# Kernel tuning notes

Hardware: AMD Instinct MI355X
Metric: run time of the kernel (lower is better)

## Reference

```python
import jax, jax.numpy as jnp
import numpy as np

EPS = 1e-5


def setup_inputs() -> dict:
    key = jax.random.key(0)
    ks = jax.random.split(key, 5)
    N, E, D, L = 10000, 160000, 512, 3
    x = jax.random.normal(ks[0], (N, D), dtype=jnp.float32)
    src = jax.random.randint(ks[1], (E,), 0, N, dtype=jnp.int64)
    dst = jax.random.randint(ks[2], (E,), 0, N, dtype=jnp.int64)
    gamma = jnp.ones((L, D), dtype=jnp.float32)
    beta = jnp.zeros((L, D), dtype=jnp.float32)
    # glorot-ish scale so ReLU stack stays well-conditioned
    W = jax.random.normal(ks[3], (L, D, D), dtype=jnp.float32) * (1.0 / np.sqrt(D))
    b = jnp.zeros((L, D), dtype=jnp.float32)
    return {"x": x, "src": src, "dst": dst, "gamma": gamma, "beta": beta, "W": W, "b": b}


def reference(x, src, dst, gamma, beta, W, b):
    N = x.shape[0]
    ones = jnp.ones(src.shape[0], dtype=x.dtype)
    # DGL GraphConv norm='both': src side uses out-degree, dst side uses in-degree
    out_deg = jnp.clip(jax.ops.segment_sum(ones, src, num_segments=N), 1.0)
    in_deg = jnp.clip(jax.ops.segment_sum(ones, dst, num_segments=N), 1.0)
    src_norm = (out_deg ** -0.5)[:, None]  # [N,1]
    dst_norm = (in_deg ** -0.5)[:, None]   # [N,1]
    n_layers = gamma.shape[0]
    for i in range(n_layers):
        # BatchNorm1d (training mode: batch mean, biased variance)
        mu = jnp.mean(x, axis=0)
        var = jnp.var(x, axis=0)
        x = (x - mu) * jax.lax.rsqrt(var + EPS) * gamma[i] + beta[i]
        h = x * src_norm
        agg = jax.ops.segment_sum(h[src], dst, num_segments=N) * dst_norm
        x = jax.nn.relu(agg @ W[i] + b[i])
    return x
```

## Files before the change

### kernel.cpp

```cpp
#include <hip/hip_runtime.h>
#include <hip/hip_bf16.h>

constexpr int N = 10000;
constexpr int D = 512;
constexpr int E = 160000;
constexpr int L = 3;
constexpr float EPS = 1e-5f;

typedef _Float16 half8 __attribute__((ext_vector_type(8)));
typedef float floatx4 __attribute__((ext_vector_type(4)));

__global__ void compute_degrees(const int* __restrict__ src,
                                const int* __restrict__ dst,
                                int* __restrict__ out_deg,
                                int* __restrict__ in_deg) {
    int e = blockIdx.x * blockDim.x + threadIdx.x;
    if (e >= E) return;
    atomicAdd(&out_deg[src[e]], 1);
    atomicAdd(&in_deg[dst[e]], 1);
}

__global__ void scan_indeg(const int* __restrict__ in_deg,
                           const int* __restrict__ out_deg,
                           int* __restrict__ off, int* __restrict__ cursor,
                           float* __restrict__ src_norm, float* __restrict__ dst_norm) {
    __shared__ int lsum[1024];
    int t = threadIdx.x;
    const int chunk = (N + 1023) / 1024;
    int start = t * chunk;
    int end = start + chunk; if (end > N) end = N;
    int s = 0;
    for (int i = start; i < end; ++i) s += in_deg[i];
    lsum[t] = s;
    __syncthreads();
    for (int d = 1; d < 1024; d <<= 1) {
        int v = (t >= d) ? lsum[t - d] : 0;
        __syncthreads();
        lsum[t] += v;
        __syncthreads();
    }
    int excl = (t == 0) ? 0 : lsum[t - 1];
    for (int i = start; i < end; ++i) {
        off[i] = excl;
        cursor[i] = excl;
        excl += in_deg[i];
        int od = out_deg[i]; if (od < 1) od = 1;
        int id = in_deg[i];  if (id < 1) id = 1;
        src_norm[i] = rsqrtf((float)od);
        dst_norm[i] = rsqrtf((float)id);
    }
    if (t == 1023) off[N] = lsum[1023];
}

__global__ void csr_fill(const int* __restrict__ src, const int* __restrict__ dst,
                         int* __restrict__ cursor, int* __restrict__ csr_src) {
    int e = blockIdx.x * blockDim.x + threadIdx.x;
    if (e >= E) return;
    int d = dst[e];
    int pos = atomicAdd(&cursor[d], 1);
    csr_src[pos] = src[e];
}

__global__ void transpose_W(const float* __restrict__ W, _Float16* __restrict__ Wt) {
    __shared__ float t[32][33];
    int l = blockIdx.z;
    int k0 = blockIdx.x * 32, n0 = blockIdx.y * 32;
    int tx = threadIdx.x, ty = threadIdx.y;
    const float* Wl = W + (size_t)l * D * D;
    _Float16* Wtl = Wt + (size_t)l * D * D;
    for (int i = 0; i < 32; i += 8)
        t[ty + i][tx] = Wl[(size_t)(k0 + ty + i) * D + n0 + tx];
    __syncthreads();
    for (int i = 0; i < 32; i += 8)
        Wtl[(size_t)(n0 + ty + i) * D + k0 + tx] = (_Float16)t[tx][ty + i];
}

__global__ void convert_x(const float* __restrict__ x, _Float16* __restrict__ y) {
    int i = blockIdx.x * 256 + threadIdx.x;
    if (i >= N * D / 8) return;
    const float* xp = x + (size_t)i * 8;
    half8 o;
    for (int k = 0; k < 8; ++k) o[k] = (_Float16)xp[k];
    *(half8*)(y + (size_t)i * 8) = o;
}

__global__ void col_stats(const _Float16* __restrict__ x, float* __restrict__ stats,
                          int rows_per_block) {
    int c = threadIdx.x;
    int r0 = blockIdx.x * rows_per_block;
    int r1 = r0 + rows_per_block; if (r1 > N) r1 = N;
    float s = 0.f, ss = 0.f;
    for (int r = r0; r < r1; ++r) {
        float v = (float)x[(size_t)r * D + c];
        s += v;
        ss += v * v;
    }
    atomicAdd(&stats[c], s);
    atomicAdd(&stats[D + c], ss);
}

__global__ void bn_coef(float* __restrict__ stats,
                        const float* __restrict__ gamma, const float* __restrict__ beta,
                        float* __restrict__ coef) {
    int c = threadIdx.x;
    const float invN = 1.0f / (float)N;
    float mu = stats[c] * invN;
    float var = stats[D + c] * invN - mu * mu;
    float scale = gamma[c] * rsqrtf(var + EPS);
    coef[c] = scale;
    coef[D + c] = beta[c] - mu * scale;
    stats[c] = 0.f;
    stats[D + c] = 0.f;
}

__global__ __launch_bounds__(256) void aggregate_bn(
    const _Float16* __restrict__ x, const int* __restrict__ off,
    const int* __restrict__ csr_src, const float* __restrict__ src_norm,
    const float* __restrict__ dst_norm, const float* __restrict__ coef,
    _Float16* __restrict__ agg) {
    int wid = (blockIdx.x * 256 + threadIdx.x) >> 6;
    if (wid >= N) return;
    int lane = threadIdx.x & 63;
    int c0 = lane * 8;
    int e0 = off[wid], e1 = off[wid + 1];
    float a[8] = {}, a2[8] = {};
    float t = 0.f;
    int e = e0;
    for (; e + 2 <= e1; e += 2) {
        int s0 = csr_src[e];
        int s1 = csr_src[e + 1];
        float n0 = src_norm[s0];
        float n1 = src_norm[s1];
        half8 v0 = *(const half8*)(x + (size_t)s0 * D + c0);
        half8 v1 = *(const half8*)(x + (size_t)s1 * D + c0);
        t += n0 + n1;
        for (int i = 0; i < 8; ++i) {
            a[i]  += (float)v0[i] * n0;
            a2[i] += (float)v1[i] * n1;
        }
    }
    if (e < e1) {
        int s0 = csr_src[e];
        float n0 = src_norm[s0];
        half8 v0 = *(const half8*)(x + (size_t)s0 * D + c0);
        t += n0;
        for (int i = 0; i < 8; ++i) a[i] += (float)v0[i] * n0;
    }
    float dn = dst_norm[wid];
    half8 o;
    for (int i = 0; i < 8; ++i) {
        float sc = coef[c0 + i];
        float sh = coef[D + c0 + i];
        o[i] = (_Float16)(dn * (sc * (a[i] + a2[i]) + sh * t));
    }
    *(half8*)(agg + (size_t)wid * D + c0) = o;
}

template <typename OutT, bool STATS>
__global__ __launch_bounds__(256) void mm_f16_relu(
    const _Float16* __restrict__ A, const _Float16* __restrict__ Bt,
    const float* __restrict__ bias, OutT* __restrict__ C, int M,
    float* __restrict__ stats) {
    __shared__ __align__(16) _Float16 As[128 * 32];
    __shared__ __align__(16) _Float16 Bs[128 * 32];
    const int tid  = threadIdx.x;
    const int wave = tid >> 6;
    const int lane = tid & 63;
    const int quad = lane >> 4;
    const int l16  = lane & 15;
    const int row0 = blockIdx.x * 128;
    const int col0 = blockIdx.y * 128;
    const int wm = (wave & 1) * 64;
    const int wn = (wave >> 1) * 64;

    const int sr = lane >> 2;
    const int sc = (lane & 3) * 8;

    floatx4 acc[4][4] = {};

    half8 pa[2], pb[2];
    for (int p = 0; p < 2; ++p) {
        int ar = row0 + wave * 32 + p * 16 + sr;
        if (ar >= M) ar = M - 1;
        pa[p] = *(const half8*)(A + (size_t)ar * D + sc);
        int br = col0 + wave * 32 + p * 16 + sr;
        pb[p] = *(const half8*)(Bt + (size_t)br * D + sc);
    }

    for (int k0 = 0; k0 < D; k0 += 32) {
        __syncthreads();
        for (int p = 0; p < 2; ++p) {
            int r = wave * 32 + p * 16 + sr;
            *(half8*)(As + r * 32 + sc) = pa[p];
            *(half8*)(Bs + r * 32 + sc) = pb[p];
        }
        __syncthreads();
        if (k0 + 32 < D) {
            int k1 = k0 + 32;
            for (int p = 0; p < 2; ++p) {
                int ar = row0 + wave * 32 + p * 16 + sr;
                if (ar >= M) ar = M - 1;
                pa[p] = *(const half8*)(A + (size_t)ar * D + k1 + sc);
                int br = col0 + wave * 32 + p * 16 + sr;
                pb[p] = *(const half8*)(Bt + (size_t)br * D + k1 + sc);
            }
        }
        half8 af[4], bf[4];
        for (int i = 0; i < 4; ++i)
            af[i] = *(const half8*)(As + (wm + i * 16 + l16) * 32 + quad * 8);
        for (int j = 0; j < 4; ++j)
            bf[j] = *(const half8*)(Bs + (wn + j * 16 + l16) * 32 + quad * 8);
        for (int i = 0; i < 4; ++i)
            for (int j = 0; j < 4; ++j)
                acc[i][j] = __builtin_amdgcn_mfma_f32_16x16x32_f16(af[i], bf[j], acc[i][j], 0, 0, 0);
    }

    float s[4] = {}, ss[4] = {};
    for (int i = 0; i < 4; ++i) {
        for (int r = 0; r < 4; ++r) {
            int row = row0 + wm + i * 16 + quad * 4 + r;
            bool valid = row < M;
            for (int j = 0; j < 4; ++j) {
                int col = col0 + wn + j * 16 + l16;
                float v = acc[i][j][r] + bias[col];
                v = v > 0.f ? v : 0.f;
                if (valid) {
                    C[(size_t)row * D + col] = (OutT)v;
                    if (STATS) { s[j] += v; ss[j] += v * v; }
                }
            }
        }
    }
    if (STATS) {
        for (int j = 0; j < 4; ++j) {
            float sv = s[j], qv = ss[j];
            sv += __shfl_xor(sv, 16); sv += __shfl_xor(sv, 32);
            qv += __shfl_xor(qv, 16); qv += __shfl_xor(qv, 32);
            if (quad == 0) {
                int col = col0 + wn + j * 16 + l16;
                atomicAdd(&stats[col], sv);
                atomicAdd(&stats[D + col], qv);
            }
        }
    }
}

extern "C" void kernel_launch(void* const* d_in, const int* in_sizes, int n_in,
                              void* d_out, int out_size, void* d_ws, size_t ws_size,
                              hipStream_t stream) {
    const float* x_in  = (const float*)d_in[0];
    const int*   src   = (const int*)d_in[1];
    const int*   dst   = (const int*)d_in[2];
    const float* gamma = (const float*)d_in[3];
    const float* beta  = (const float*)d_in[4];
    const float* W     = (const float*)d_in[5];
    const float* b     = (const float*)d_in[6];
    float* out = (float*)d_out;

    char* p = (char*)d_ws;
    _Float16* x16 = (_Float16*)p;  p += (size_t)N * D * 2;
    _Float16* agg = (_Float16*)p;  p += (size_t)N * D * 2;
    _Float16* Wt  = (_Float16*)p;  p += (size_t)L * D * D * 2;
    float* coef     = (float*)p;   p += 2 * D * 4;
    float* src_norm = (float*)p;   p += (size_t)N * 4;
    float* dst_norm = (float*)p;   p += (size_t)N * 4;
    int* out_deg = (int*)p;        p += (size_t)N * 4;
    int* in_deg  = (int*)p;        p += (size_t)N * 4;
    float* stats = (float*)p;      p += 2 * D * 4;
    int* csr_off = (int*)p;        p += (size_t)(N + 1) * 4;
    int* cursor  = (int*)p;        p += (size_t)N * 4;
    int* csr_src = (int*)p;        p += (size_t)E * 4;

    hipMemsetAsync(out_deg, 0, (2 * (size_t)N + 2 * D) * sizeof(int), stream);
    compute_degrees<<<(E + 255) / 256, 256, 0, stream>>>(src, dst, out_deg, in_deg);
    scan_indeg<<<1, 1024, 0, stream>>>(in_deg, out_deg, csr_off, cursor, src_norm, dst_norm);
    csr_fill<<<(E + 255) / 256, 256, 0, stream>>>(src, dst, cursor, csr_src);
    transpose_W<<<dim3(16, 16, 3), dim3(32, 8), 0, stream>>>(W, Wt);
    convert_x<<<(N * D / 8 + 255) / 256, 256, 0, stream>>>(x_in, x16);
    col_stats<<<100, D, 0, stream>>>(x16, stats, (N + 99) / 100);

    dim3 mm_grid((N + 127) / 128, D / 128);
    const int agg_blocks = (N + 3) / 4;

    for (int l = 0; l < L; ++l) {
        const float* gl  = gamma + (size_t)l * D;
        const float* bl  = beta + (size_t)l * D;
        const _Float16* Wl = Wt + (size_t)l * D * D;
        const float* bil = b + (size_t)l * D;

        bn_coef<<<1, D, 0, stream>>>(stats, gl, bl, coef);
        aggregate_bn<<<agg_blocks, 256, 0, stream>>>(x16, csr_off, csr_src,
                                                     src_norm, dst_norm, coef, agg);
        if (l == L - 1) {
            mm_f16_relu<float, false><<<mm_grid, 256, 0, stream>>>(
                agg, Wl, bil, out, N, nullptr);
        } else {
            mm_f16_relu<_Float16, true><<<mm_grid, 256, 0, stream>>>(
                agg, Wl, bil, x16, N, stats);
        }
    }
}
```

Baseline: 311.0 us.

## Fuse setup kernels, fold BN coefficients into aggregation, use direct-to-LDS GEMM loads

The degree count, x conversion with fused column stats, and W transpose now run as one combined setup kernel. Column stats are computed from the fp32 input, and per-layer stats buffers remove the bn_coef launch, since aggregation now derives the BN scale and shift inline. The GEMM tile shrinks to 128x64 and uses global_load_lds to copy tiles straight into shared memory instead of prefetching through registers. Together these cut kernel launches and register staging. The cost is that the GEMM no longer overlaps the next tile's loads with MFMA work, and the smaller tile adds grid blocks and more A re-reads.

```diff
diff --git a/kernel.cpp b/kernel.cpp
--- a/kernel.cpp
+++ b/kernel.cpp
@@ -8,16 +8,67 @@
 constexpr float EPS = 1e-5f;
 
 typedef _Float16 half8 __attribute__((ext_vector_type(8)));
+typedef _Float16 half2v __attribute__((ext_vector_type(2)));
 typedef float floatx4 __attribute__((ext_vector_type(4)));
 
-__global__ void compute_degrees(const int* __restrict__ src,
-                                const int* __restrict__ dst,
-                                int* __restrict__ out_deg,
-                                int* __restrict__ in_deg) {
-    int e = blockIdx.x * blockDim.x + threadIdx.x;
-    if (e >= E) return;
-    atomicAdd(&out_deg[src[e]], 1);
-    atomicAdd(&in_deg[dst[e]], 1);
+__device__ __forceinline__ void glds16(const _Float16* g, _Float16* l) {
+    __builtin_amdgcn_global_load_lds(
+        (const __attribute__((address_space(1))) uint32_t*)(g),
+        (__attribute__((address_space(3))) uint32_t*)(l),
+        16, 0, 0);
+}
+
+constexpr int DEG_BLOCKS  = (E + 255) / 256;
+constexpr int CONV_BLOCKS = 100;
+constexpr int TW_BLOCKS   = L * 256;
+constexpr int MEGA_BLOCKS = DEG_BLOCKS + CONV_BLOCKS + TW_BLOCKS;
+
+__global__ __launch_bounds__(256) void mega_setup(
+    const int* __restrict__ src, const int* __restrict__ dst,
+    const float* __restrict__ x, const float* __restrict__ W,
+    int* __restrict__ out_deg, int* __restrict__ in_deg,
+    _Float16* __restrict__ x16, float* __restrict__ stats0,
+    _Float16* __restrict__ Wt) {
+    __shared__ float tb[32][33];
+    int bid = blockIdx.x;
+    int tid = threadIdx.x;
+    if (bid < DEG_BLOCKS) {
+        int e = bid * 256 + tid;
+        if (e < E) {
+            atomicAdd(&out_deg[src[e]], 1);
+            atomicAdd(&in_deg[dst[e]], 1);
+        }
+    } else if (bid < DEG_BLOCKS + CONV_BLOCKS) {
+        int b = bid - DEG_BLOCKS;
+        int r0 = b * 100;
+        int r1 = r0 + 100; if (r1 > N) r1 = N;
+        int c2 = tid * 2;
+        float s0 = 0.f, s1 = 0.f, q0 = 0.f, q1 = 0.f;
+        for (int r = r0; r < r1; ++r) {
+            float2 v = *(const float2*)(x + (size_t)r * D + c2);
+            s0 += v.x; q0 += v.x * v.x;
+            s1 += v.y; q1 += v.y * v.y;
+            half2v h; h[0] = (_Float16)v.x; h[1] = (_Float16)v.y;
+            *(half2v*)(x16 + (size_t)r * D + c2) = h;
+        }
+        atomicAdd(&stats0[c2], s0);
+        atomicAdd(&stats0[c2 + 1], s1);
+        atomicAdd(&stats0[D + c2], q0);
+        atomicAdd(&stats0[D + c2 + 1], q1);
+    } else {
+        int b = bid - DEG_BLOCKS - CONV_BLOCKS;
+        int l = b >> 8;
+        int t = b & 255;
+        int k0 = (t >> 4) * 32, n0 = (t & 15) * 32;
+        int tx = tid & 31, ty = tid >> 5;
+        const float* Wl = W + (size_t)l * D * D;
+        _Float16* Wtl = Wt + (size_t)l * D * D;
+        for (int i = 0; i < 32; i += 8)
+            tb[ty + i][tx] = Wl[(size_t)(k0 + ty + i) * D + n0 + tx];
+        __syncthreads();
+        for (int i = 0; i < 32; i += 8)
+            Wtl[(size_t)(n0 + ty + i) * D + k0 + tx] = (_Float16)tb[tx][ty + i];
+    }
 }
 
 __global__ void scan_indeg(const int* __restrict__ in_deg,
@@ -61,67 +112,28 @@
     csr_src[pos] = src[e];
 }
 
-__global__ void transpose_W(const float* __restrict__ W, _Float16* __restrict__ Wt) {
-    __shared__ float t[32][33];
-    int l = blockIdx.z;
-    int k0 = blockIdx.x * 32, n0 = blockIdx.y * 32;
-    int tx = threadIdx.x, ty = threadIdx.y;
-    const float* Wl = W + (size_t)l * D * D;
-    _Float16* Wtl = Wt + (size_t)l * D * D;
-    for (int i = 0; i < 32; i += 8)
-        t[ty + i][tx] = Wl[(size_t)(k0 + ty + i) * D + n0 + tx];
-    __syncthreads();
-    for (int i = 0; i < 32; i += 8)
-        Wtl[(size_t)(n0 + ty + i) * D + k0 + tx] = (_Float16)t[tx][ty + i];
-}
-
-__global__ void convert_x(const float* __restrict__ x, _Float16* __restrict__ y) {
-    int i = blockIdx.x * 256 + threadIdx.x;
-    if (i >= N * D / 8) return;
-    const float* xp = x + (size_t)i * 8;
-    half8 o;
-    for (int k = 0; k < 8; ++k) o[k] = (_Float16)xp[k];
-    *(half8*)(y + (size_t)i * 8) = o;
-}
-
-__global__ void col_stats(const _Float16* __restrict__ x, float* __restrict__ stats,
-                          int rows_per_block) {
-    int c = threadIdx.x;
-    int r0 = blockIdx.x * rows_per_block;
-    int r1 = r0 + rows_per_block; if (r1 > N) r1 = N;
-    float s = 0.f, ss = 0.f;
-    for (int r = r0; r < r1; ++r) {
-        float v = (float)x[(size_t)r * D + c];
-        s += v;
-        ss += v * v;
-    }
-    atomicAdd(&stats[c], s);
-    atomicAdd(&stats[D + c], ss);
-}
-
-__global__ void bn_coef(float* __restrict__ stats,
-                        const float* __restrict__ gamma, const float* __restrict__ beta,
-                        float* __restrict__ coef) {
-    int c = threadIdx.x;
-    const float invN = 1.0f / (float)N;
-    float mu = stats[c] * invN;
-    float var = stats[D + c] * invN - mu * mu;
-    float scale = gamma[c] * rsqrtf(var + EPS);
-    coef[c] = scale;
-    coef[D + c] = beta[c] - mu * scale;
-    stats[c] = 0.f;
-    stats[D + c] = 0.f;
-}
-
 __global__ __launch_bounds__(256) void aggregate_bn(
     const _Float16* __restrict__ x, const int* __restrict__ off,
     const int* __restrict__ csr_src, const float* __restrict__ src_norm,
-    const float* __restrict__ dst_norm, const float* __restrict__ coef,
+    const float* __restrict__ dst_norm, const float* __restrict__ stats,
+    const float* __restrict__ gamma, const float* __restrict__ beta,
     _Float16* __restrict__ agg) {
     int wid = (blockIdx.x * 256 + threadIdx.x) >> 6;
     if (wid >= N) return;
     int lane = threadIdx.x & 63;
     int c0 = lane * 8;
+
+    float scale[8], shift[8];
+    const float invN = 1.0f / (float)N;
+    for (int i = 0; i < 8; ++i) {
+        int c = c0 + i;
+        float mu = stats[c] * invN;
+        float var = stats[D + c] * invN - mu * mu;
+        float sc = gamma[c] * rsqrtf(var + EPS);
+        scale[i] = sc;
+        shift[i] = beta[c] - mu * sc;
+    }
+
     int e0 = off[wid], e1 = off[wid + 1];
     float a[8] = {}, a2[8] = {};
     float t = 0.f;
@@ -148,11 +160,8 @@
     }
     float dn = dst_norm[wid];
     half8 o;
-    for (int i = 0; i < 8; ++i) {
-        float sc = coef[c0 + i];
-        float sh = coef[D + c0 + i];
-        o[i] = (_Float16)(dn * (sc * (a[i] + a2[i]) + sh * t));
-    }
+    for (int i = 0; i < 8; ++i)
+        o[i] = (_Float16)(dn * (scale[i] * (a[i] + a2[i]) + shift[i] * t));
     *(half8*)(agg + (size_t)wid * D + c0) = o;
 }
 
@@ -162,78 +171,67 @@
     const float* __restrict__ bias, OutT* __restrict__ C, int M,
     float* __restrict__ stats) {
     __shared__ __align__(16) _Float16 As[128 * 32];
-    __shared__ __align__(16) _Float16 Bs[128 * 32];
+    __shared__ __align__(16) _Float16 Bs[64 * 32];
     const int tid  = threadIdx.x;
     const int wave = tid >> 6;
     const int lane = tid & 63;
     const int quad = lane >> 4;
     const int l16  = lane & 15;
     const int row0 = blockIdx.x * 128;
-    const int col0 = blockIdx.y * 128;
+    const int col0 = blockIdx.y * 64;
     const int wm = (wave & 1) * 64;
-    const int wn = (wave >> 1) * 64;
-
+    const int wn = (wave >> 1) * 32;
     const int sr = lane >> 2;
     const int sc = (lane & 3) * 8;
 
-    floatx4 acc[4][4] = {};
-
-    half8 pa[2], pb[2];
-    for (int p = 0; p < 2; ++p) {
-        int ar = row0 + wave * 32 + p * 16 + sr;
-        if (ar >= M) ar = M - 1;
-        pa[p] = *(const half8*)(A + (size_t)ar * D + sc);
-        int br = col0 + wave * 32 + p * 16 + sr;
-        pb[p] = *(const half8*)(Bt + (size_t)br * D + sc);
-    }
+    int ar0 = row0 + wave * 32 + sr;
+    int ar1 = ar0 + 16;
+    if (ar0 >= M) ar0 = M - 1;
+    if (ar1 >= M) ar1 = M - 1;
+    const _Float16* gA0 = A + (size_t)ar0 * D + sc;
+    const _Float16* gA1 = A + (size_t)ar1 * D + sc;
+    const _Float16* gB  = Bt + (size_t)(col0 + wave * 16 + sr) * D + sc;
+    _Float16* lA0 = As + (wave * 32) * 32;
+    _Float16* lA1 = As + (wave * 32 + 16) * 32;
+    _Float16* lB  = Bs + (wave * 16) * 32;
+
+    floatx4 acc[4][2] = {};
 
     for (int k0 = 0; k0 < D; k0 += 32) {
         __syncthreads();
-        for (int p = 0; p < 2; ++p) {
-            int r = wave * 32 + p * 16 + sr;
-            *(half8*)(As + r * 32 + sc) = pa[p];
-            *(half8*)(Bs + r * 32 + sc) = pb[p];
-        }
-        __syncthreads();
-        if (k0 + 32 < D) {
-            int k1 = k0 + 32;
-            for (int p = 0; p < 2; ++p) {
-                int ar = row0 + wave * 32 + p * 16 + sr;
-                if (ar >= M) ar = M - 1;
-                pa[p] = *(const half8*)(A + (size_t)ar * D + k1 + sc);
-                int br = col0 + wave * 32 + p * 16 + sr;
-                pb[p] = *(const half8*)(Bt + (size_t)br * D + k1 + sc);
-            }
-        }
-        half8 af[4], bf[4];
+        glds16(gA0 + k0, lA0);
+        glds16(gA1 + k0, lA1);
+        glds16(gB + k0, lB);
+        __syncthreads();
+        half8 af[4], bf[2];
         for (int i = 0; i < 4; ++i)
             af[i] = *(const half8*)(As + (wm + i * 16 + l16) * 32 + quad * 8);
-        for (int j = 0; j < 4; ++j)
+        for (int j = 0; j < 2; ++j)
             bf[j] = *(const half8*)(Bs + (wn + j * 16 + l16) * 32 + quad * 8);
         for (int i = 0; i < 4; ++i)
-            for (int j = 0; j < 4; ++j)
+            for (int j = 0; j < 2; ++j)
                 acc[i][j] = __builtin_amdgcn_mfma_f32_16x16x32_f16(af[i], bf[j], acc[i][j], 0, 0, 0);
     }
 
-    float s[4] = {}, ss[4] = {};
+    float s[2] = {}, q[2] = {};
     for (int i = 0; i < 4; ++i) {
         for (int r = 0; r < 4; ++r) {
             int row = row0 + wm + i * 16 + quad * 4 + r;
             bool valid = row < M;
-            for (int j = 0; j < 4; ++j) {
+            for (int j = 0; j < 2; ++j) {
                 int col = col0 + wn + j * 16 + l16;
                 float v = acc[i][j][r] + bias[col];
                 v = v > 0.f ? v : 0.f;
                 if (valid) {
                     C[(size_t)row * D + col] = (OutT)v;
-                    if (STATS) { s[j] += v; ss[j] += v * v; }
+                    if (STATS) { s[j] += v; q[j] += v * v; }
                 }
             }
         }
     }
     if (STATS) {
-        for (int j = 0; j < 4; ++j) {
-            float sv = s[j], qv = ss[j];
+        for (int j = 0; j < 2; ++j) {
+            float sv = s[j], qv = q[j];
             sv += __shfl_xor(sv, 16); sv += __shfl_xor(sv, 32);
             qv += __shfl_xor(qv, 16); qv += __shfl_xor(qv, 32);
             if (quad == 0) {
@@ -261,25 +259,27 @@
     _Float16* x16 = (_Float16*)p;  p += (size_t)N * D * 2;
     _Float16* agg = (_Float16*)p;  p += (size_t)N * D * 2;
     _Float16* Wt  = (_Float16*)p;  p += (size_t)L * D * D * 2;
-    float* coef     = (float*)p;   p += 2 * D * 4;
     float* src_norm = (float*)p;   p += (size_t)N * 4;
     float* dst_norm = (float*)p;   p += (size_t)N * 4;
-    int* out_deg = (int*)p;        p += (size_t)N * 4;
-    int* in_deg  = (int*)p;        p += (size_t)N * 4;
-    float* stats = (float*)p;      p += 2 * D * 4;
-    int* csr_off = (int*)p;        p += (size_t)(N + 1) * 4;
-    int* cursor  = (int*)p;        p += (size_t)N * 4;
-    int* csr_src = (int*)p;        p += (size_t)E * 4;
-
-    hipMemsetAsync(out_deg, 0, (2 * (size_t)N + 2 * D) * sizeof(int), stream);
-    compute_degrees<<<(E + 255) / 256, 256, 0, stream>>>(src, dst, out_deg, in_deg);
-    scan_indeg<<<1, 1024, 0, stream>>>(in_deg, out_deg, csr_off, cursor, src_norm, dst_norm);
-    csr_fill<<<(E + 255) / 256, 256, 0, stream>>>(src, dst, cursor, csr_src);
-    transpose_W<<<dim3(16, 16, 3), dim3(32, 8), 0, stream>>>(W, Wt);
-    convert_x<<<(N * D / 8 + 255) / 256, 256, 0, stream>>>(x_in, x16);
-    col_stats<<<100, D, 0, stream>>>(x16, stats, (N + 99) / 100);
-
-    dim3 mm_grid((N + 127) / 128, D / 128);
+    int* out_deg   = (int*)p;      p += (size_t)N * 4;
+    int* in_deg    = (int*)p;      p += (size_t)N * 4;
+    float* stats0  = (float*)p;    p += 2 * D * 4;
+    float* stats1  = (float*)p;    p += 2 * D * 4;
+    float* stats2  = (float*)p;    p += 2 * D * 4;
+    int* csr_off   = (int*)p;      p += (size_t)(N + 1) * 4;
+    int* cursor    = (int*)p;      p += (size_t)N * 4;
+    int* csr_src   = (int*)p;      p += (size_t)E * 4;
+
+    float* stats_in[3] = {stats0, stats1, stats2};
+
+    hipMemsetAsync(out_deg, 0, (2 * (size_t)N + 6 * D) * sizeof(int), stream);
+    mega_setup<<<MEGA_BLOCKS, 256, 0, stream>>>(src, dst, x_in, W,
+                                                out_deg, in_deg, x16, stats0, Wt);
+    scan_indeg<<<1, 1024, 0, stream>>>(in_deg, out_deg, csr_off, cursor,
+                                       src_norm, dst_norm);
+    csr_fill<<<DEG_BLOCKS, 256, 0, stream>>>(src, dst, cursor, csr_src);
+
+    dim3 mm_grid((N + 127) / 128, D / 64);
     const int agg_blocks = (N + 3) / 4;
 
     for (int l = 0; l < L; ++l) {
@@ -288,15 +288,14 @@
         const _Float16* Wl = Wt + (size_t)l * D * D;
         const float* bil = b + (size_t)l * D;
 
-        bn_coef<<<1, D, 0, stream>>>(stats, gl, bl, coef);
-        aggregate_bn<<<agg_blocks, 256, 0, stream>>>(x16, csr_off, csr_src,
-                                                     src_norm, dst_norm, coef, agg);
+        aggregate_bn<<<agg_blocks, 256, 0, stream>>>(
+            x16, csr_off, csr_src, src_norm, dst_norm, stats_in[l], gl, bl, agg);
         if (l == L - 1) {
             mm_f16_relu<float, false><<<mm_grid, 256, 0, stream>>>(
                 agg, Wl, bil, out, N, nullptr);
         } else {
             mm_f16_relu<_Float16, true><<<mm_grid, 256, 0, stream>>>(
-                agg, Wl, bil, x16, N, stats);
-        }
-    }
-}
+                agg, Wl, bil, x16, N, stats_in[l + 1]);
+        }
+    }
+}
```

Measured after the change: 282.5 us. 1.1x faster.
